# Kernel optimization log

Measured on AMD Instinct MI355X. Metric: run time of the kernel, lower is better.

## Reference

```python
import jax, jax.numpy as jnp
import numpy as np

EPS = 1e-7  # K.epsilon()
ROUTINGS = 3
NUM_CAPS = 24
DIM_CAPS = 128


def squash(x, axis=-1):
    # NOTE: this repo's squash is x / sqrt(||x||^2 + eps)  (NOT the standard capsule squash)
    s = jnp.sum(jnp.square(x), axis=axis, keepdims=True)
    return x / jnp.sqrt(s + EPS)


def setup_inputs() -> dict:
    key = jax.random.key(0)
    k1, k2 = jax.random.split(key)
    B, N_IN, D_IN = 16, 1024, 256
    u_vecs = jax.random.normal(k1, (B, N_IN, D_IN), dtype=jnp.float32)
    # glorot-ish scale for the shared 1x1-conv kernel, flattened to [D_IN, NUM_CAPS*DIM_CAPS]
    W = jax.random.normal(k2, (D_IN, NUM_CAPS * DIM_CAPS), dtype=jnp.float32) * 0.02
    return {"u_vecs": u_vecs, "W": W}


def reference(u_vecs, W):
    B, N_in, _ = u_vecs.shape
    # shared-weight K.conv1d with kernel size 1 == matmul over last dim
    u_hat = jnp.einsum("bni,io->bno", u_vecs, W)
    u_hat = u_hat.reshape(B, N_in, NUM_CAPS, DIM_CAPS).transpose(0, 2, 1, 3)  # [B,K,N,D]

    b = jnp.zeros((B, NUM_CAPS, N_in), dtype=u_hat.dtype)
    outputs = None
    for i in range(ROUTINGS):
        c = jax.nn.softmax(b, axis=1)                         # softmax over capsule axis
        s = jnp.einsum("bkn,bknd->bkd", c, u_hat)             # weighted sum over input caps
        outputs = squash(s, axis=-1)                          # [B,K,D]
        if i < ROUTINGS - 1:
            b = jnp.einsum("bkd,bknd->bkn", outputs, u_hat)   # agreement update
    return outputs
```

## Files before the change

### kernel.cpp

```cpp
#include <hip/hip_runtime.h>

#define B_ 16
#define N_ 1024
#define DIN 256
#define K_ 24
#define D_ 128
#define KD_ 3072
#define NSPLIT 16
#define NCHUNK 64
#define EPS_ 1e-7f
#define NBLK 256
#define NUNIT (B_ * K_)

__device__ __forceinline__ float cload(const float* p) {
    return __hip_atomic_load(p, __ATOMIC_RELAXED, __HIP_MEMORY_SCOPE_AGENT);
}
__device__ __forceinline__ void cstore(float* p, float v) {
    __hip_atomic_store(p, v, __ATOMIC_RELAXED, __HIP_MEMORY_SCOPE_AGENT);
}

__device__ __forceinline__ unsigned* F1p(unsigned* f, int j, int b) {
    return f + (j * 16 + b) * 16;
}
__device__ __forceinline__ unsigned* F2p(unsigned* f, int j, int b) {
    return f + 768 + (j * 16 + b) * 16;
}
__device__ __forceinline__ void flag_add(unsigned* f) {
    asm volatile("" ::: "memory");
    __hip_atomic_fetch_add(f, 1u, __ATOMIC_RELAXED, __HIP_MEMORY_SCOPE_AGENT);
}
__device__ __forceinline__ void flag_wait(unsigned* f, unsigned target) {
    while (__hip_atomic_load(f, __ATOMIC_RELAXED, __HIP_MEMORY_SCOPE_AGENT) < target)
        __builtin_amdgcn_s_sleep(1);
    asm volatile("" ::: "memory");
}

__device__ __forceinline__ void sv_phase(int iter, int beta, int t,
                                         const float* __restrict__ W,
                                         const float* __restrict__ tupart,
                                         const float* __restrict__ tpart,
                                         float* __restrict__ w2,
                                         float* __restrict__ out,
                                         float* Rbuf, unsigned* flg) {
    float* t_lds = Rbuf;
    float* v_lds = Rbuf + 256;
    float* sred  = Rbuf + 512;
    float* red2  = Rbuf + 1024;
    for (int unit = beta; unit < NUNIT; unit += NBLK) {
        const int b = unit / K_, k = unit % K_;
        if (t == 0) flag_wait(F1p(flg, iter, b), 16);
        __syncthreads();
        if (t < DIN) {
            float a = 0.f;
            if (iter == 0) {
                #pragma unroll
                for (int s2 = 0; s2 < NSPLIT; ++s2)
                    a += cload(tupart + ((size_t)(b * NSPLIT + s2)) * DIN + t);
                a *= (1.0f / 24.0f);
            } else {
                #pragma unroll
                for (int s2 = 0; s2 < NSPLIT; ++s2)
                    a += cload(tpart + ((size_t)((b * NSPLIT + s2) * K_ + k)) * DIN + t);
            }
            t_lds[t] = a;
        }
        __syncthreads();
        {
            const int d = t & (D_ - 1), q = t >> 7;
            const float* Wp = W + (size_t)(q * 64) * KD_ + (size_t)k * D_ + d;
            const float* tp = t_lds + q * 64;
            float sd = 0.f;
            #pragma unroll 8
            for (int i = 0; i < 64; ++i) sd += tp[i] * Wp[(size_t)i * KD_];
            sred[q * D_ + d] = sd;
        }
        __syncthreads();
        float sd = 0.f;
        if (t < D_) {
            sd = (sred[t] + sred[D_ + t]) + (sred[2 * D_ + t] + sred[3 * D_ + t]);
            float sq = sd * sd;
            #pragma unroll
            for (int m = 1; m < 64; m <<= 1) sq += __shfl_xor(sq, m);
            if ((t & 63) == 0) red2[t >> 6] = sq;
        }
        __syncthreads();
        const float inv = rsqrtf(red2[0] + red2[1] + EPS_);
        if (t < D_) {
            const float vd = sd * inv;
            v_lds[t] = vd;
            if (iter == 2) out[((size_t)(b * K_ + k)) * D_ + t] = vd;
        }
        __syncthreads();
        if (iter != 2) {
            if (t < DIN) {
                const float4* Wq = (const float4*)(W + (size_t)t * KD_ + (size_t)k * D_);
                const float4* vq = (const float4*)v_lds;
                float a = 0.f;
                #pragma unroll 8
                for (int q2 = 0; q2 < 32; ++q2) {
                    float4 wv = Wq[q2], vv = vq[q2];
                    a += wv.x * vv.x + wv.y * vv.y + wv.z * vv.z + wv.w * vv.w;
                }
                cstore(w2 + ((size_t)(b * K_ + k)) * DIN + t, a);
            }
            __syncthreads();
            if (t == 0) flag_add(F2p(flg, iter, b));
        }
    }
}

__device__ __forceinline__ void fused_phase(int iter, int b, int s, int t,
                                            const float* __restrict__ w2,
                                            float* __restrict__ tpart,
                                            const float* u_lds, float* Rbuf,
                                            float* c_lds, float* w2_lds,
                                            unsigned* flg) {
    if (t == 0) flag_wait(F2p(flg, iter - 1, b), 24);
    __syncthreads();
    {
        const float* w2g = w2 + (size_t)b * K_ * DIN;
        for (int idx = t; idx < K_ * DIN; idx += 512)
            w2_lds[idx] = cload(w2g + idx);
    }
    __syncthreads();

    {
        const int npair = t & 31, ipart = t >> 5;
        const int n0 = npair * 2, i0 = ipart * 16;
        float acc0[K_], acc1[K_];
        #pragma unroll
        for (int k = 0; k < K_; ++k) { acc0[k] = 0.f; acc1[k] = 0.f; }
        #pragma unroll
        for (int g = 0; g < 4; ++g) {
            float ua0[4], ua1[4];
            #pragma unroll
            for (int m = 0; m < 4; ++m) {
                ua0[m] = u_lds[(n0 + 0) * 257 + i0 + g * 4 + m];
                ua1[m] = u_lds[(n0 + 1) * 257 + i0 + g * 4 + m];
            }
            #pragma unroll
            for (int k = 0; k < K_; ++k) {
                const float4 wq = *(const float4*)(w2_lds + k * DIN + i0 + g * 4);
                acc0[k] += ua0[0] * wq.x + ua0[1] * wq.y + ua0[2] * wq.z + ua0[3] * wq.w;
                acc1[k] += ua1[0] * wq.x + ua1[1] * wq.y + ua1[2] * wq.z + ua1[3] * wq.w;
            }
        }
        #pragma unroll
        for (int k = 0; k < K_; ++k) {
            acc0[k] += __shfl_xor(acc0[k], 32);
            acc1[k] += __shfl_xor(acc1[k], 32);
        }
        const int w = t >> 6;
        const int hi = (t & 63) >= 32;
        float* sc = Rbuf + (w * NCHUNK + n0 + (hi ? 1 : 0)) * 25;
        #pragma unroll
        for (int k = 0; k < K_; ++k) sc[k] = hi ? acc1[k] : acc0[k];
    }
    __syncthreads();

    {
        const int n = t >> 3, kq = t & 7;
        float lg[3];
        #pragma unroll
        for (int j = 0; j < 3; ++j) {
            float a = 0.f;
            #pragma unroll
            for (int w = 0; w < 8; ++w) a += Rbuf[(w * NCHUNK + n) * 25 + kq * 3 + j];
            lg[j] = a;
        }
        float mx = fmaxf(fmaxf(lg[0], lg[1]), lg[2]);
        #pragma unroll
        for (int m = 1; m < 8; m <<= 1) mx = fmaxf(mx, __shfl_xor(mx, m));
        float e0 = __expf(lg[0] - mx), e1 = __expf(lg[1] - mx), e2 = __expf(lg[2] - mx);
        float sm = e0 + e1 + e2;
        #pragma unroll
        for (int m = 1; m < 8; m <<= 1) sm += __shfl_xor(sm, m);
        const float inv = 1.0f / sm;
        c_lds[n * 32 + kq * 3 + 0] = e0 * inv;
        c_lds[n * 32 + kq * 3 + 1] = e1 * inv;
        c_lds[n * 32 + kq * 3 + 2] = e2 * inv;
    }
    __syncthreads();

    {
        const int i = t & 255, nh = t >> 8;
        float acc[K_];
        #pragma unroll
        for (int k = 0; k < K_; ++k) acc[k] = 0.f;
        #pragma unroll 4
        for (int n = nh * 32; n < nh * 32 + 32; ++n) {
            const float uv = u_lds[n * 257 + i];
            const float4* cq = (const float4*)(c_lds + n * 32);
            #pragma unroll
            for (int q = 0; q < 6; ++q) {
                float4 cv = cq[q];
                acc[q * 4 + 0] += uv * cv.x;
                acc[q * 4 + 1] += uv * cv.y;
                acc[q * 4 + 2] += uv * cv.z;
                acc[q * 4 + 3] += uv * cv.w;
            }
        }
        __syncthreads();
        if (nh == 1) {
            #pragma unroll
            for (int k = 0; k < K_; ++k) Rbuf[k * 257 + i] = acc[k];
        }
        __syncthreads();
        if (nh == 0) {
            float* tp = tpart + ((size_t)((b * NSPLIT + s) * K_)) * DIN + i;
            #pragma unroll
            for (int k = 0; k < K_; ++k)
                cstore(tp + (size_t)k * DIN, acc[k] + Rbuf[k * 257 + i]);
        }
    }
    __syncthreads();
    if (t == 0) flag_add(F1p(flg, iter, b));
}

__global__ __launch_bounds__(512, 1) void k_caps(const float* __restrict__ u,
                                                 const float* __restrict__ W,
                                                 float* __restrict__ out,
                                                 float* __restrict__ tupart,
                                                 float* __restrict__ tpart,
                                                 float* __restrict__ w2,
                                                 unsigned* __restrict__ flg) {
    const int beta = blockIdx.x;
    const int b = beta >> 4, s = beta & 15;
    const int t = threadIdx.x;

    __shared__ float u_lds[NCHUNK * 257];
    __shared__ __align__(16) float Rbuf[12800];
    __shared__ __align__(16) float c_lds[NCHUNK * 32];
    __shared__ __align__(16) float w2_lds[K_ * DIN];

    {
        const float4* ug = (const float4*)(u + ((size_t)(b * N_ + s * NCHUNK)) * DIN);
        for (int idx = t; idx < NCHUNK * 64; idx += 512) {
            const int n = idx >> 6, q = idx & 63;
            float4 v = ug[(size_t)n * 64 + q];
            float* dst = u_lds + n * 257 + q * 4;
            dst[0] = v.x; dst[1] = v.y; dst[2] = v.z; dst[3] = v.w;
        }
        __syncthreads();
        if (t < DIN) {
            float a = 0.f;
            #pragma unroll
            for (int n = 0; n < NCHUNK; ++n) a += u_lds[n * 257 + t];
            cstore(tupart + ((size_t)(b * NSPLIT + s)) * DIN + t, a);
        }
        __syncthreads();
        if (t == 0) flag_add(F1p(flg, 0, b));
    }

    sv_phase(0, beta, t, W, tupart, tpart, w2, out, Rbuf, flg);
    fused_phase(1, b, s, t, w2, tpart, u_lds, Rbuf, c_lds, w2_lds, flg);
    sv_phase(1, beta, t, W, tupart, tpart, w2, out, Rbuf, flg);
    fused_phase(2, b, s, t, w2, tpart, u_lds, Rbuf, c_lds, w2_lds, flg);
    sv_phase(2, beta, t, W, tupart, tpart, w2, out, Rbuf, flg);
}

extern "C" void kernel_launch(void* const* d_in, const int* in_sizes, int n_in,
                              void* d_out, int out_size, void* d_ws, size_t ws_size,
                              hipStream_t stream) {
    const float* u = (const float*)d_in[0];
    const float* W = (const float*)d_in[1];
    float* out = (float*)d_out;

    char* ws = (char*)d_ws;
    float* tpart    = (float*)ws;
    float* w2       = (float*)(ws + 6291456);
    float* tupart   = (float*)(ws + 6291456 + 393216);
    unsigned* flg   = (unsigned*)(ws + 6946816);

    hipMemsetAsync(flg, 0, 6144, stream);

    void* args[] = {(void*)&u, (void*)&W, (void*)&out,
                    (void*)&tupart, (void*)&tpart, (void*)&w2, (void*)&flg};
    hipLaunchCooperativeKernel(reinterpret_cast<void*>(k_caps),
                               dim3(NBLK), dim3(512), args, 0, stream);
}
```

Baseline: 102.0 us.

## Double block size to 1024 threads and re-split work across all phases

Launches 1024 threads per block instead of 512 and reworks each phase to use the extra threads. The s·W reduction is split eight ways and the W·v dot product four ways with shuffles. The logit/softmax stage is restructured so 16 lanes per input capsule reduce via shuffles, which drops the large LDS scratch buffer and two barriers. The c·u accumulation is split by capsule group instead of by n-halves, removing a cross-half LDS reduction. The flag increment now uses release ordering, which may add a cache writeback cost but makes the cross-block synchronisation safer. The aim is more parallelism per block and a shorter serial dependency chain, at the cost of higher register pressure with 1024 threads.

```diff
diff --git a/kernel.cpp b/kernel.cpp
--- a/kernel.cpp
+++ b/kernel.cpp
@@ -27,7 +27,7 @@
 }
 __device__ __forceinline__ void flag_add(unsigned* f) {
     asm volatile("" ::: "memory");
-    __hip_atomic_fetch_add(f, 1u, __ATOMIC_RELAXED, __HIP_MEMORY_SCOPE_AGENT);
+    __hip_atomic_fetch_add(f, 1u, __ATOMIC_RELEASE, __HIP_MEMORY_SCOPE_AGENT);
 }
 __device__ __forceinline__ void flag_wait(unsigned* f, unsigned target) {
     while (__hip_atomic_load(f, __ATOMIC_RELAXED, __HIP_MEMORY_SCOPE_AGENT) < target)
@@ -41,11 +41,11 @@
                                          const float* __restrict__ tpart,
                                          float* __restrict__ w2,
                                          float* __restrict__ out,
-                                         float* Rbuf, unsigned* flg) {
-    float* t_lds = Rbuf;
-    float* v_lds = Rbuf + 256;
-    float* sred  = Rbuf + 512;
-    float* red2  = Rbuf + 1024;
+                                         float* shbuf, unsigned* flg) {
+    float* t_lds = shbuf;
+    float* sred  = shbuf + 256;
+    float* red2  = shbuf + 1280;
+    float* v_lds = shbuf + 1284;
     for (int unit = beta; unit < NUNIT; unit += NBLK) {
         const int b = unit / K_, k = unit % K_;
         if (t == 0) flag_wait(F1p(flg, iter, b), 16);
@@ -67,17 +67,18 @@
         __syncthreads();
         {
             const int d = t & (D_ - 1), q = t >> 7;
-            const float* Wp = W + (size_t)(q * 64) * KD_ + (size_t)k * D_ + d;
-            const float* tp = t_lds + q * 64;
+            const float* Wp = W + (size_t)(q * 32) * KD_ + (size_t)k * D_ + d;
+            const float* tp = t_lds + q * 32;
             float sd = 0.f;
             #pragma unroll 8
-            for (int i = 0; i < 64; ++i) sd += tp[i] * Wp[(size_t)i * KD_];
+            for (int i = 0; i < 32; ++i) sd += tp[i] * Wp[(size_t)i * KD_];
             sred[q * D_ + d] = sd;
         }
         __syncthreads();
         float sd = 0.f;
         if (t < D_) {
-            sd = (sred[t] + sred[D_ + t]) + (sred[2 * D_ + t] + sred[3 * D_ + t]);
+            #pragma unroll
+            for (int q = 0; q < 8; ++q) sd += sred[q * D_ + t];
             float sq = sd * sd;
             #pragma unroll
             for (int m = 1; m < 64; m <<= 1) sq += __shfl_xor(sq, m);
@@ -92,17 +93,18 @@
         }
         __syncthreads();
         if (iter != 2) {
-            if (t < DIN) {
-                const float4* Wq = (const float4*)(W + (size_t)t * KD_ + (size_t)k * D_);
-                const float4* vq = (const float4*)v_lds;
-                float a = 0.f;
-                #pragma unroll 8
-                for (int q2 = 0; q2 < 32; ++q2) {
-                    float4 wv = Wq[q2], vv = vq[q2];
-                    a += wv.x * vv.x + wv.y * vv.y + wv.z * vv.z + wv.w * vv.w;
-                }
-                cstore(w2 + ((size_t)(b * K_ + k)) * DIN + t, a);
+            const int i = t >> 2, dq = t & 3;
+            const float4* Wq = (const float4*)(W + (size_t)i * KD_ + (size_t)k * D_ + dq * 32);
+            const float4* vq = (const float4*)(v_lds + dq * 32);
+            float a = 0.f;
+            #pragma unroll
+            for (int m = 0; m < 8; ++m) {
+                float4 wv = Wq[m], vv = vq[m];
+                a += wv.x * vv.x + wv.y * vv.y + wv.z * vv.z + wv.w * vv.w;
             }
+            a += __shfl_xor(a, 1);
+            a += __shfl_xor(a, 2);
+            if (dq == 0) cstore(w2 + ((size_t)(b * K_ + k)) * DIN + i, a);
             __syncthreads();
             if (t == 0) flag_add(F2p(flg, iter, b));
         }
@@ -112,130 +114,95 @@
 __device__ __forceinline__ void fused_phase(int iter, int b, int s, int t,
                                             const float* __restrict__ w2,
                                             float* __restrict__ tpart,
-                                            const float* u_lds, float* Rbuf,
-                                            float* c_lds, float* w2_lds,
-                                            unsigned* flg) {
+                                            const float* u_lds, float* shbuf,
+                                            float* w2_lds, unsigned* flg) {
     if (t == 0) flag_wait(F2p(flg, iter - 1, b), 24);
     __syncthreads();
     {
         const float* w2g = w2 + (size_t)b * K_ * DIN;
-        for (int idx = t; idx < K_ * DIN; idx += 512)
-            w2_lds[idx] = cload(w2g + idx);
-    }
-    __syncthreads();
-
-    {
-        const int npair = t & 31, ipart = t >> 5;
-        const int n0 = npair * 2, i0 = ipart * 16;
-        float acc0[K_], acc1[K_];
-        #pragma unroll
-        for (int k = 0; k < K_; ++k) { acc0[k] = 0.f; acc1[k] = 0.f; }
+        #pragma unroll
+        for (int r = 0; r < 6; ++r)
+            w2_lds[t + r * 1024] = cload(w2g + t + r * 1024);
+    }
+    __syncthreads();
+
+    float* c_lds = shbuf;
+    {
+        const int n = t >> 4, p = t & 15;
+        float acc[K_];
+        #pragma unroll
+        for (int k = 0; k < K_; ++k) acc[k] = 0.f;
         #pragma unroll
         for (int g = 0; g < 4; ++g) {
-            float ua0[4], ua1[4];
-            #pragma unroll
-            for (int m = 0; m < 4; ++m) {
-                ua0[m] = u_lds[(n0 + 0) * 257 + i0 + g * 4 + m];
-                ua1[m] = u_lds[(n0 + 1) * 257 + i0 + g * 4 + m];
+            const int i0 = p * 4 + g * 64;
+            const float ua0 = u_lds[n * 257 + i0 + 0];
+            const float ua1 = u_lds[n * 257 + i0 + 1];
+            const float ua2 = u_lds[n * 257 + i0 + 2];
+            const float ua3 = u_lds[n * 257 + i0 + 3];
+            #pragma unroll
+            for (int k = 0; k < K_; ++k) {
+                const float4 wq = *(const float4*)(w2_lds + k * DIN + i0);
+                acc[k] += ua0 * wq.x + ua1 * wq.y + ua2 * wq.z + ua3 * wq.w;
             }
-            #pragma unroll
-            for (int k = 0; k < K_; ++k) {
-                const float4 wq = *(const float4*)(w2_lds + k * DIN + i0 + g * 4);
-                acc0[k] += ua0[0] * wq.x + ua0[1] * wq.y + ua0[2] * wq.z + ua0[3] * wq.w;
-                acc1[k] += ua1[0] * wq.x + ua1[1] * wq.y + ua1[2] * wq.z + ua1[3] * wq.w;
-            }
-        }
-        #pragma unroll
-        for (int k = 0; k < K_; ++k) {
-            acc0[k] += __shfl_xor(acc0[k], 32);
-            acc1[k] += __shfl_xor(acc1[k], 32);
-        }
-        const int w = t >> 6;
-        const int hi = (t & 63) >= 32;
-        float* sc = Rbuf + (w * NCHUNK + n0 + (hi ? 1 : 0)) * 25;
-        #pragma unroll
-        for (int k = 0; k < K_; ++k) sc[k] = hi ? acc1[k] : acc0[k];
-    }
-    __syncthreads();
-
-    {
-        const int n = t >> 3, kq = t & 7;
-        float lg[3];
-        #pragma unroll
-        for (int j = 0; j < 3; ++j) {
-            float a = 0.f;
-            #pragma unroll
-            for (int w = 0; w < 8; ++w) a += Rbuf[(w * NCHUNK + n) * 25 + kq * 3 + j];
-            lg[j] = a;
-        }
-        float mx = fmaxf(fmaxf(lg[0], lg[1]), lg[2]);
-        #pragma unroll
-        for (int m = 1; m < 8; m <<= 1) mx = fmaxf(mx, __shfl_xor(mx, m));
-        float e0 = __expf(lg[0] - mx), e1 = __expf(lg[1] - mx), e2 = __expf(lg[2] - mx);
-        float sm = e0 + e1 + e2;
-        #pragma unroll
-        for (int m = 1; m < 8; m <<= 1) sm += __shfl_xor(sm, m);
+        }
+        #pragma unroll
+        for (int m = 1; m < 16; m <<= 1)
+            #pragma unroll
+            for (int k = 0; k < K_; ++k) acc[k] += __shfl_xor(acc[k], m);
+        float mx = acc[0];
+        #pragma unroll
+        for (int k = 1; k < K_; ++k) mx = fmaxf(mx, acc[k]);
+        float sm = 0.f;
+        #pragma unroll
+        for (int k = 0; k < K_; ++k) { acc[k] = __expf(acc[k] - mx); sm += acc[k]; }
         const float inv = 1.0f / sm;
-        c_lds[n * 32 + kq * 3 + 0] = e0 * inv;
-        c_lds[n * 32 + kq * 3 + 1] = e1 * inv;
-        c_lds[n * 32 + kq * 3 + 2] = e2 * inv;
-    }
-    __syncthreads();
-
-    {
-        const int i = t & 255, nh = t >> 8;
-        float acc[K_];
-        #pragma unroll
-        for (int k = 0; k < K_; ++k) acc[k] = 0.f;
+        if (p < 8) {
+            c_lds[n * 28 + p * 3 + 0] = acc[p * 3 + 0] * inv;
+            c_lds[n * 28 + p * 3 + 1] = acc[p * 3 + 1] * inv;
+            c_lds[n * 28 + p * 3 + 2] = acc[p * 3 + 2] * inv;
+        }
+    }
+    __syncthreads();
+
+    {
+        const int i = t & 255, kg = t >> 8;
+        float a0 = 0.f, a1 = 0.f, a2 = 0.f, a3 = 0.f, a4 = 0.f, a5 = 0.f;
         #pragma unroll 4
-        for (int n = nh * 32; n < nh * 32 + 32; ++n) {
+        for (int n = 0; n < NCHUNK; ++n) {
             const float uv = u_lds[n * 257 + i];
-            const float4* cq = (const float4*)(c_lds + n * 32);
-            #pragma unroll
-            for (int q = 0; q < 6; ++q) {
-                float4 cv = cq[q];
-                acc[q * 4 + 0] += uv * cv.x;
-                acc[q * 4 + 1] += uv * cv.y;
-                acc[q * 4 + 2] += uv * cv.z;
-                acc[q * 4 + 3] += uv * cv.w;
-            }
-        }
-        __syncthreads();
-        if (nh == 1) {
-            #pragma unroll
-            for (int k = 0; k < K_; ++k) Rbuf[k * 257 + i] = acc[k];
-        }
-        __syncthreads();
-        if (nh == 0) {
-            float* tp = tpart + ((size_t)((b * NSPLIT + s) * K_)) * DIN + i;
-            #pragma unroll
-            for (int k = 0; k < K_; ++k)
-                cstore(tp + (size_t)k * DIN, acc[k] + Rbuf[k * 257 + i]);
-        }
+            const float* cr = c_lds + n * 28 + kg * 6;
+            a0 += uv * cr[0]; a1 += uv * cr[1]; a2 += uv * cr[2];
+            a3 += uv * cr[3]; a4 += uv * cr[4]; a5 += uv * cr[5];
+        }
+        float* tp = tpart + ((size_t)((b * NSPLIT + s) * K_ + kg * 6)) * DIN + i;
+        cstore(tp + 0 * DIN, a0); cstore(tp + 1 * DIN, a1);
+        cstore(tp + 2 * DIN, a2); cstore(tp + 3 * DIN, a3);
+        cstore(tp + 4 * DIN, a4); cstore(tp + 5 * DIN, a5);
     }
     __syncthreads();
     if (t == 0) flag_add(F1p(flg, iter, b));
 }
 
-__global__ __launch_bounds__(512, 1) void k_caps(const float* __restrict__ u,
-                                                 const float* __restrict__ W,
-                                                 float* __restrict__ out,
-                                                 float* __restrict__ tupart,
-                                                 float* __restrict__ tpart,
-                                                 float* __restrict__ w2,
-                                                 unsigned* __restrict__ flg) {
+__global__ __launch_bounds__(1024, 4) void k_caps(const float* __restrict__ u,
+                                                  const float* __restrict__ W,
+                                                  float* __restrict__ out,
+                                                  float* __restrict__ tupart,
+                                                  float* __restrict__ tpart,
+                                                  float* __restrict__ w2,
+                                                  unsigned* __restrict__ flg) {
     const int beta = blockIdx.x;
     const int b = beta >> 4, s = beta & 15;
     const int t = threadIdx.x;
 
     __shared__ float u_lds[NCHUNK * 257];
-    __shared__ __align__(16) float Rbuf[12800];
-    __shared__ __align__(16) float c_lds[NCHUNK * 32];
     __shared__ __align__(16) float w2_lds[K_ * DIN];
+    __shared__ __align__(16) float shbuf[1792];
 
     {
         const float4* ug = (const float4*)(u + ((size_t)(b * N_ + s * NCHUNK)) * DIN);
-        for (int idx = t; idx < NCHUNK * 64; idx += 512) {
+        #pragma unroll
+        for (int r = 0; r < 4; ++r) {
+            const int idx = t + r * 1024;
             const int n = idx >> 6, q = idx & 63;
             float4 v = ug[(size_t)n * 64 + q];
             float* dst = u_lds + n * 257 + q * 4;
@@ -252,11 +219,11 @@
         if (t == 0) flag_add(F1p(flg, 0, b));
     }
 
-    sv_phase(0, beta, t, W, tupart, tpart, w2, out, Rbuf, flg);
-    fused_phase(1, b, s, t, w2, tpart, u_lds, Rbuf, c_lds, w2_lds, flg);
-    sv_phase(1, beta, t, W, tupart, tpart, w2, out, Rbuf, flg);
-    fused_phase(2, b, s, t, w2, tpart, u_lds, Rbuf, c_lds, w2_lds, flg);
-    sv_phase(2, beta, t, W, tupart, tpart, w2, out, Rbuf, flg);
+    sv_phase(0, beta, t, W, tupart, tpart, w2, out, shbuf, flg);
+    fused_phase(1, b, s, t, w2, tpart, u_lds, shbuf, w2_lds, flg);
+    sv_phase(1, beta, t, W, tupart, tpart, w2, out, shbuf, flg);
+    fused_phase(2, b, s, t, w2, tpart, u_lds, shbuf, w2_lds, flg);
+    sv_phase(2, beta, t, W, tupart, tpart, w2, out, shbuf, flg);
 }
 
 extern "C" void kernel_launch(void* const* d_in, const int* in_sizes, int n_in,
@@ -277,5 +244,5 @@
     void* args[] = {(void*)&u, (void*)&W, (void*)&out,
                     (void*)&tupart, (void*)&tpart, (void*)&w2, (void*)&flg};
     hipLaunchCooperativeKernel(reinterpret_cast<void*>(k_caps),
-                               dim3(NBLK), dim3(512), args, 0, stream);
-}
+                               dim3(NBLK), dim3(1024), args, 0, stream);
+}
```

Result: slower. 125.8 us (+23.3%).
